# Performance work log

Hardware: AMD Instinct MI355X
Metric: run time of the kernel (lower is better)

## Reference

```python
import jax, jax.numpy as jnp
import numpy as np

N_SRC_F = 40000; N_TGT_F = 40000; N_F = N_SRC_F + N_TGT_F
N_SRC_C = 1024; N_TGT_C = 1024; N_C = N_SRC_C + N_TGT_C
NN = 30        # KPConv neighbors per point
K = 15         # kernel points
C1 = 128       # fine-level feats (first_feats_dim)
C2 = 256       # coarse encoder out dim
GNN = 256      # gnn_feats_dim
HEADS = 4
DGCNN_K = 10
FINAL = 32     # final_feats_dim
EXT_F = 1.0; EXT_C = 2.0   # KPConv influence extents (scaled to unit-cube clouds)
EPS = 1e-12


def kpconv(q_pts, s_pts, s_feats, neighb, kpts, W, extent):
    # q_pts [Nq,3], s_pts [Ns,3], s_feats [Ns,Cin], neighb [Nq,NN], kpts [K,3], W [K,Cin,Cout]
    npts = s_pts[neighb]                              # [Nq,NN,3] irregular gather
    rel = npts - q_pts[:, None, :]
    # ||rel - kp||^2 expanded to avoid a [Nq,NN,K,3] intermediate
    d2 = (jnp.sum(rel * rel, -1)[:, :, None] + jnp.sum(kpts * kpts, -1)[None, None, :]
          - 2.0 * jnp.einsum('njd,kd->njk', rel, kpts))
    infl = jax.nn.relu(1.0 - jnp.sqrt(jnp.maximum(d2, EPS)) / extent)   # [Nq,NN,K]
    nf = s_feats[neighb]                              # [Nq,NN,Cin]
    h = jnp.einsum('njk,njc->nkc', infl, nf)          # kernel-point aggregation
    return jnp.einsum('nkc,kcd->nd', h, W)


def knn_idx(coords, k):
    sq = jnp.sum(coords * coords, -1)
    d2 = sq[:, None] + sq[None, :] - 2.0 * (coords @ coords.T)
    return jax.lax.top_k(-d2, k)[1]


def self_layer(coords, x, W, b):
    # DGCNN edge conv: knn on coords, edge = [x_i, x_j - x_i], 1x1 conv + relu, max over k
    idx = knn_idx(coords, DGCNN_K)
    neigh = x[idx]                                    # [N,k,C]
    ctr = jnp.broadcast_to(x[:, None, :], neigh.shape)
    edge = jnp.concatenate([ctr, neigh - ctr], -1)    # [N,k,2C]
    return jnp.max(jax.nn.relu(edge @ W + b), axis=1)


def cross_layer(x, y, Wq, Wk, Wv, Wm, bm):
    # multi-head cross attention x <- y, residual MLP on [x, message]
    N, C = x.shape
    dh = C // HEADS
    q = (x @ Wq).reshape(N, HEADS, dh)
    k = (y @ Wk).reshape(-1, HEADS, dh)
    v = (y @ Wv).reshape(-1, HEADS, dh)
    attn = jax.nn.softmax(jnp.einsum('nhd,mhd->hnm', q, k) / float(np.sqrt(dh)), axis=-1)
    msg = jnp.einsum('hnm,mhd->nhd', attn, v).reshape(N, C)
    return x + jnp.concatenate([x, msg], -1) @ Wm + bm


def l2norm(x):
    return x / jnp.maximum(jnp.linalg.norm(x, axis=1, keepdims=True), EPS)


def _forward(points_f, points_c, features, kernel_points_f, kernel_points_c,
             W_kp1, W_kp2, W_bottle, b_bottle, W_self1, b_self1,
             Wq, Wk, Wv, W_cross, b_cross, W_self2, b_self2,
             W_proj, b_proj, W_score, b_score, epsilon, W_dec, b_dec,
             neighbors_f, pool_idx, upsample_idx, len_src_c):
    # --- encoder: fine KPConv + strided KPConv to coarse ---
    x_f = kpconv(points_f, points_f, features, neighbors_f, kernel_points_f, W_kp1, EXT_F)  # [N_f,C1]
    skip = x_f
    x_c = kpconv(points_c, points_f, x_f, pool_idx, kernel_points_c, W_kp2, EXT_C)          # [N_c,C2]
    feats_c = x_c @ W_bottle + b_bottle                # bottleneck 1x1 conv -> [N_c,GNN]
    src, tgt = feats_c[:len_src_c], feats_c[len_src_c:]
    sc, tc = points_c[:len_src_c], points_c[len_src_c:]
    # --- GCN: self -> cross -> self (weights shared across src/tgt) ---
    src = self_layer(sc, src, W_self1, b_self1)
    tgt = self_layer(tc, tgt, W_self1, b_self1)
    src2 = cross_layer(src, tgt, Wq, Wk, Wv, W_cross, b_cross)
    tgt2 = cross_layer(tgt, src, Wq, Wk, Wv, W_cross, b_cross)
    src = self_layer(sc, src2, W_self2, b_self2)
    tgt = self_layer(tc, tgt2, W_self2, b_self2)
    feats = jnp.concatenate([src, tgt], 0) @ W_proj + b_proj   # proj_gnn
    scores_c_raw = feats @ W_score + b_score                   # proj_score [N_c,1]
    feats_norm = l2norm(feats)
    # --- bidirectional temperature-softmax matching head ---
    ip = feats_norm[:len_src_c] @ feats_norm[len_src_c:].T     # [Ns,Nt]
    temperature = jnp.exp(epsilon) + 0.03
    s1 = jax.nn.softmax(ip / temperature, axis=1) @ scores_c_raw[len_src_c:]
    s2 = jax.nn.softmax(ip.T / temperature, axis=1) @ scores_c_raw[:len_src_c]
    scores_saliency = jnp.concatenate([s1, s2], 0)
    # condition=True, add_cross_overlap=True branch
    x = jnp.concatenate([scores_c_raw, scores_saliency, feats], 1)    # [N_c, GNN+2]
    # --- decoder: nearest upsample + skip concat + unary conv ---
    x = jnp.concatenate([x[upsample_idx], skip], 1)            # [N_f, GNN+2+C1]
    x = x @ W_dec + b_dec                                      # [N_f, FINAL+2]
    feats_f = l2norm(x[:, :FINAL])
    so = jnp.clip(jax.nn.sigmoid(x[:, FINAL]), 0.0, 1.0)
    ss = jnp.clip(jax.nn.sigmoid(x[:, FINAL + 1]), 0.0, 1.0)
    so = jnp.where(jnp.isnan(so) | jnp.isinf(so), 0.0, so)     # regular_score
    ss = jnp.where(jnp.isnan(ss) | jnp.isinf(ss), 0.0, ss)
    return feats_f, so, ss


def _p(k, shape, fan):
    return jax.random.normal(k, shape, jnp.float32) / float(np.sqrt(fan))


def setup_inputs() -> dict:
    key = jax.random.key(0)
    ks = jax.random.split(key, 24)
    inp = {}
    inp['points_f'] = jax.random.uniform(ks[0], (N_F, 3), jnp.float32)
    inp['points_c'] = jax.random.uniform(ks[1], (N_C, 3), jnp.float32)
    inp['features'] = jnp.ones((N_F, 1), jnp.float32)
    inp['kernel_points_f'] = jax.random.normal(ks[2], (K, 3), jnp.float32) * 0.3
    inp['kernel_points_c'] = jax.random.normal(ks[3], (K, 3), jnp.float32) * 0.6
    inp['W_kp1'] = _p(ks[4], (K, 1, C1), K)
    inp['W_kp2'] = _p(ks[5], (K, C1, C2), K * C1)
    inp['W_bottle'] = _p(ks[6], (C2, GNN), C2); inp['b_bottle'] = jnp.zeros((GNN,), jnp.float32)
    inp['W_self1'] = _p(ks[7], (2 * GNN, GNN), 2 * GNN); inp['b_self1'] = jnp.zeros((GNN,), jnp.float32)
    inp['Wq'] = _p(ks[8], (GNN, GNN), GNN)
    inp['Wk'] = _p(ks[9], (GNN, GNN), GNN)
    inp['Wv'] = _p(ks[10], (GNN, GNN), GNN)
    inp['W_cross'] = _p(ks[11], (2 * GNN, GNN), 2 * GNN); inp['b_cross'] = jnp.zeros((GNN,), jnp.float32)
    inp['W_self2'] = _p(ks[12], (2 * GNN, GNN), 2 * GNN); inp['b_self2'] = jnp.zeros((GNN,), jnp.float32)
    inp['W_proj'] = _p(ks[13], (GNN, GNN), GNN); inp['b_proj'] = jnp.zeros((GNN,), jnp.float32)
    inp['W_score'] = _p(ks[14], (GNN, 1), GNN); inp['b_score'] = jnp.zeros((1,), jnp.float32)
    inp['epsilon'] = jnp.array(-5.0, jnp.float32)
    inp['W_dec'] = _p(ks[15], (GNN + 2 + C1, FINAL + 2), GNN + 2 + C1); inp['b_dec'] = jnp.zeros((FINAL + 2,), jnp.float32)
    inp['neighbors_f'] = jax.random.randint(ks[16], (N_F, NN), 0, N_F)
    inp['pool_idx'] = jax.random.randint(ks[17], (N_C, NN), 0, N_F)
    inp['upsample_idx'] = jax.random.randint(ks[18], (N_F,), 0, N_C)
    inp['len_src_c'] = N_SRC_C
    inp['len_src_f'] = N_SRC_F
    return inp


def reference(points_f, points_c, features, kernel_points_f, kernel_points_c,
              W_kp1, W_kp2, W_bottle, b_bottle, W_self1, b_self1,
              Wq, Wk, Wv, W_cross, b_cross, W_self2, b_self2,
              W_proj, b_proj, W_score, b_score, epsilon, W_dec, b_dec,
              neighbors_f, pool_idx, upsample_idx, len_src_c, len_src_f):
    return _forward(points_f, points_c, features, kernel_points_f, kernel_points_c,
                    W_kp1, W_kp2, W_bottle, b_bottle, W_self1, b_self1,
                    Wq, Wk, Wv, W_cross, b_cross, W_self2, b_self2,
                    W_proj, b_proj, W_score, b_score, epsilon, W_dec, b_dec,
                    neighbors_f, pool_idx, upsample_idx, len_src_c)
```

## Files before the change

### kernel.cpp

```cpp
#include <hip/hip_runtime.h>
#include <math.h>

#define NFINE   80000
#define NCRS    2048
#define NSRC    1024
#define NNB     30
#define KP      15
#define C1D     128
#define C2D     256
#define GD      256
#define DGK     10
#define FINALD  32
#define DECOUT  34

#define NCHUNK  8
#define CHUNK   128
#define TK      8
#define KC      4
#define KSTEP   480
#define GTR     16

__global__ __launch_bounds__(256) void kpconv_fine(
    const float* __restrict__ pts, const float* __restrict__ feat,
    const int* __restrict__ nbr, const float* __restrict__ kp,
    const float* __restrict__ W, float* __restrict__ out)
{
    int t = threadIdx.x, w = t >> 6, lane = t & 63;
    int n = blockIdx.x * 4 + w;
    __shared__ float contrib[4][NNB][17];
    __shared__ float h[4][KP + 1];
    float kx[KP], ky[KP], kz[KP], kk[KP];
#pragma unroll
    for (int k = 0; k < KP; k++) {
        kx[k] = kp[k*3]; ky[k] = kp[k*3+1]; kz[k] = kp[k*3+2];
        kk[k] = kx[k]*kx[k] + ky[k]*ky[k] + kz[k]*kz[k];
    }
    if (lane < NNB) {
        float qx = pts[n*3], qy = pts[n*3+1], qz = pts[n*3+2];
        int id = nbr[n*NNB + lane];
        float rx = pts[id*3]-qx, ry = pts[id*3+1]-qy, rz = pts[id*3+2]-qz;
        float rr = rx*rx + ry*ry + rz*rz;
        float f = feat[id];
#pragma unroll
        for (int k = 0; k < KP; k++) {
            float d2 = rr + kk[k] - 2.f*(rx*kx[k] + ry*ky[k] + rz*kz[k]);
            float infl = fmaxf(1.f - sqrtf(fmaxf(d2, 1e-12f)), 0.f);
            contrib[w][lane][k] = infl * f;
        }
    }
    __syncthreads();
    if (lane < KP) {
        float s = 0.f;
#pragma unroll
        for (int j = 0; j < NNB; j++) s += contrib[w][j][lane];
        h[w][lane] = s;
    }
    __syncthreads();
    float a0 = 0.f, a1 = 0.f;
#pragma unroll
    for (int k = 0; k < KP; k++) {
        float hk = h[w][k];
        a0 += hk * W[k*C1D + lane];
        a1 += hk * W[k*C1D + 64 + lane];
    }
    out[(size_t)n*C1D + lane]      = a0;
    out[(size_t)n*C1D + 64 + lane] = a1;
}

__global__ __launch_bounds__(256) void hh_kernel(
    const float* __restrict__ pc, const float* __restrict__ pf,
    const float* __restrict__ xf, const int* __restrict__ pool,
    const float* __restrict__ kp, float* __restrict__ hhg)
{
    int n = blockIdx.x, t = threadIdx.x;
    __shared__ float kx[KP], ky[KP], kz[KP], kk[KP];
    __shared__ float rel[NNB][4];
    __shared__ int   ids[NNB];
    __shared__ float infl[NNB][KP + 1];
    __shared__ float nf[NNB][C1D];
    if (t < KP) {
        float a = kp[t*3], b = kp[t*3+1], c = kp[t*3+2];
        kx[t] = a; ky[t] = b; kz[t] = c; kk[t] = a*a + b*b + c*c;
    }
    if (t < NNB) {
        int id = pool[n*NNB + t]; ids[t] = id;
        float qx = pc[n*3], qy = pc[n*3+1], qz = pc[n*3+2];
        float rx = pf[id*3]-qx, ry = pf[id*3+1]-qy, rz = pf[id*3+2]-qz;
        rel[t][0] = rx; rel[t][1] = ry; rel[t][2] = rz;
        rel[t][3] = rx*rx + ry*ry + rz*rz;
    }
    __syncthreads();
    for (int i = t; i < NNB*KP; i += 256) {
        int j = i / KP, kq = i % KP;
        float d2 = rel[j][3] + kk[kq]
                 - 2.f*(rel[j][0]*kx[kq] + rel[j][1]*ky[kq] + rel[j][2]*kz[kq]);
        infl[j][kq] = fmaxf(1.f - sqrtf(fmaxf(d2, 1e-12f)) * 0.5f, 0.f);
    }
    for (int i = t; i < NNB*C1D; i += 256) {
        int j = i >> 7, c = i & 127;
        nf[j][c] = xf[(size_t)ids[j]*C1D + c];
    }
    __syncthreads();
    for (int i = t; i < KP*C1D; i += 256) {
        int kq = i >> 7, c = i & 127;
        float s = 0.f;
#pragma unroll
        for (int j = 0; j < NNB; j++) s += infl[j][kq] * nf[j][c];
        hhg[(size_t)n*(KP*C1D) + i] = s;
    }
}

__global__ __launch_bounds__(256) void hh_gemm(
    const float* __restrict__ hhg, const float* __restrict__ W,
    float* __restrict__ pbuf)
{
    int t = threadIdx.x;
    int rg = blockIdx.x >> 2, kc = blockIdx.x & 3;
    int n0 = rg * GTR, kb0 = kc * KSTEP;
    __shared__ float xi[GTR][KSTEP];
    float* xf = &xi[0][0];
    for (int i = t; i < GTR*KSTEP; i += 256) {
        int r = i / KSTEP, c = i - r*KSTEP;
        xf[i] = hhg[(size_t)(n0 + r)*(KP*C1D) + kb0 + c];
    }
    __syncthreads();
    float a[GTR];
#pragma unroll
    for (int r = 0; r < GTR; r++) a[r] = 0.f;
    for (int c = 0; c < KSTEP; c += 4) {
        float w0 = W[(size_t)(kb0+c+0)*C2D + t];
        float w1 = W[(size_t)(kb0+c+1)*C2D + t];
        float w2 = W[(size_t)(kb0+c+2)*C2D + t];
        float w3 = W[(size_t)(kb0+c+3)*C2D + t];
#pragma unroll
        for (int r = 0; r < GTR; r++) {
            float4 xv = *(const float4*)&xi[r][c];
            a[r] += xv.x*w0 + xv.y*w1 + xv.z*w2 + xv.w*w3;
        }
    }
#pragma unroll
    for (int r = 0; r < GTR; r++)
        pbuf[(size_t)kc*NCRS*C2D + (size_t)(n0+r)*C2D + t] = a[r];
}

__global__ __launch_bounds__(256) void bottle_fused(
    const float* __restrict__ pbuf, const float* __restrict__ Wb,
    const float* __restrict__ b, float* __restrict__ out)
{
    int t = threadIdx.x, n0 = blockIdx.x * 4;
    const size_t MN = (size_t)NCRS*C2D;
    __shared__ float xi[4][C2D];
    for (int i = t; i < 4*C2D; i += 256) {
        int r = i >> 8, c = i & 255;
        size_t off = (size_t)(n0+r)*C2D + c;
        xi[r][c] = pbuf[off] + pbuf[MN+off] + pbuf[2*MN+off] + pbuf[3*MN+off];
    }
    __syncthreads();
    float a[4];
#pragma unroll
    for (int r = 0; r < 4; r++) a[r] = 0.f;
    for (int c = 0; c < C2D; c += 4) {
        float w0 = Wb[(c+0)*GD + t];
        float w1 = Wb[(c+1)*GD + t];
        float w2 = Wb[(c+2)*GD + t];
        float w3 = Wb[(c+3)*GD + t];
#pragma unroll
        for (int r = 0; r < 4; r++) {
            float4 xv = *(const float4*)&xi[r][c];
            a[r] += xv.x*w0 + xv.y*w1 + xv.z*w2 + xv.w*w3;
        }
    }
    float bv = b[t];
#pragma unroll
    for (int r = 0; r < 4; r++) out[(size_t)(n0+r)*GD + t] = a[r] + bv;
}

__global__ __launch_bounds__(512) void self_gemm(
    const float* __restrict__ x, const float* __restrict__ W,
    float* __restrict__ Y)
{
    int t = threadIdx.x, n0 = blockIdx.x * 4;
    __shared__ float xi[4][GD];
    for (int i = t; i < 4*GD; i += 512) {
        int r = i >> 8, c = i & 255;
        xi[r][c] = x[(size_t)(n0+r)*GD + c];
    }
    __syncthreads();
    const float* wcol = (t < GD) ? (W + t) : (W + (size_t)GD*GD + (t - GD));
    float a[4];
#pragma unroll
    for (int r = 0; r < 4; r++) a[r] = 0.f;
    for (int c = 0; c < GD; c += 4) {
        float w0 = wcol[(size_t)(c+0)*GD];
        float w1 = wcol[(size_t)(c+1)*GD];
        float w2 = wcol[(size_t)(c+2)*GD];
        float w3 = wcol[(size_t)(c+3)*GD];
#pragma unroll
        for (int r = 0; r < 4; r++) {
            float4 xv = *(const float4*)&xi[r][c];
            a[r] += xv.x*w0 + xv.y*w1 + xv.z*w2 + xv.w*w3;
        }
    }
#pragma unroll
    for (int r = 0; r < 4; r++) Y[(size_t)(n0+r)*512 + t] = a[r];
}

__global__ __launch_bounds__(256) void edge_max(
    const float* __restrict__ Y, const int* __restrict__ knn,
    const float* __restrict__ b, float* __restrict__ out)
{
    int n = blockIdx.x, t = threadIdx.x;
    int base = (n < NSRC) ? 0 : NSRC;
    __shared__ int ids[DGK];
    if (t < DGK) ids[t] = base + knn[n*DGK + t];
    __syncthreads();
    float a  = Y[(size_t)n*512 + t];
    float bn = Y[(size_t)n*512 + GD + t];
    float cst = a - bn + b[t];
    float acc = 0.f;
#pragma unroll
    for (int j = 0; j < DGK; j++) {
        float bj = Y[(size_t)ids[j]*512 + GD + t];
        acc = fmaxf(acc, fmaxf(cst + bj, 0.f));
    }
    out[(size_t)n*GD + t] = acc;
}

__global__ __launch_bounds__(256) void qkv_kernel(
    const float* __restrict__ x, const float* __restrict__ Wq,
    const float* __restrict__ Wk, const float* __restrict__ Wv,
    float* __restrict__ qb, float* __restrict__ kb, float* __restrict__ vb)
{
    int t = threadIdx.x, n0 = blockIdx.x * 4;
    __shared__ float xi[4][GD];
    for (int i = t; i < 4*GD; i += 256) {
        int r = i >> 8, c = i & 255;
        xi[r][c] = x[(size_t)(n0+r)*GD + c];
    }
    __syncthreads();
    const float* Ws[3] = {Wq, Wk, Wv};
    float* outs[3] = {qb, kb, vb};
#pragma unroll
    for (int m = 0; m < 3; m++) {
        const float* W = Ws[m];
        float a[4];
#pragma unroll
        for (int r = 0; r < 4; r++) a[r] = 0.f;
        for (int c = 0; c < GD; c += 4) {
            float w0 = W[(c+0)*GD + t];
            float w1 = W[(c+1)*GD + t];
            float w2 = W[(c+2)*GD + t];
            float w3 = W[(c+3)*GD + t];
#pragma unroll
            for (int r = 0; r < 4; r++) {
                float4 xv = *(const float4*)&xi[r][c];
                a[r] += xv.x*w0 + xv.y*w1 + xv.z*w2 + xv.w*w3;
            }
        }
        float* o = outs[m];
#pragma unroll
        for (int r = 0; r < 4; r++) o[(size_t)(n0+r)*GD + t] = a[r];
    }
}

__global__ __launch_bounds__(256) void knn_kernel(
    const float* __restrict__ pts, int* __restrict__ knn)
{
    int g = blockIdx.x;
    int t = threadIdx.x;
    int base = (g < NSRC) ? 0 : NSRC;
    int local = g - base;
    const float* P = pts + (size_t)base*3;
    __shared__ float d2s[NSRC];
    __shared__ float wval[4];
    __shared__ int   widx[4];
    float qx = P[local*3], qy = P[local*3+1], qz = P[local*3+2];
    float sqn = qx*qx + qy*qy + qz*qz;
#pragma unroll
    for (int ii = 0; ii < 4; ii++) {
        int m = t + ii*256;
        float px = P[m*3], py = P[m*3+1], pz = P[m*3+2];
        float sqm = px*px + py*py + pz*pz;
        d2s[m] = sqn + sqm - 2.f*(qx*px + qy*py + qz*pz);
    }
    __syncthreads();
    for (int r = 0; r < DGK; r++) {
        float bv = 3.4e38f; int bidx = NSRC;
#pragma unroll
        for (int ii = 0; ii < 4; ii++) {
            int m = t + ii*256;
            float v = d2s[m];
            if (v < bv) { bv = v; bidx = m; }
        }
#pragma unroll
        for (int off = 32; off >= 1; off >>= 1) {
            float ov = __shfl_xor(bv, off);
            int   oi = __shfl_xor(bidx, off);
            if (ov < bv || (ov == bv && oi < bidx)) { bv = ov; bidx = oi; }
        }
        if ((t & 63) == 0) { wval[t >> 6] = bv; widx[t >> 6] = bidx; }
        __syncthreads();
        if (t == 0) {
            float fv = wval[0]; int fi = widx[0];
#pragma unroll
            for (int wv2 = 1; wv2 < 4; wv2++)
                if (wval[wv2] < fv || (wval[wv2] == fv && widx[wv2] < fi)) {
                    fv = wval[wv2]; fi = widx[wv2];
                }
            knn[g*DGK + r] = fi;
            d2s[fi] = 3.4e38f;
        }
        __syncthreads();
    }
}

__global__ __launch_bounds__(256) void attn_flash(
    const float* __restrict__ qb, const float* __restrict__ kb,
    const float* __restrict__ vb, float* __restrict__ pm,
    float* __restrict__ pl, float* __restrict__ pacc)
{
    int bidx = blockIdx.x;
    int h = bidx & 3, chunk = (bidx >> 2) & 7, rb = bidx >> 5;
    int t = threadIdx.x;
    int u = t >> 3, li = t & 7;
    int row0 = rb * 128 + u * 4;
    int kbase = (row0 < NSRC) ? NSRC : 0;

    __shared__ float4 kt[2][TK][16];
    __shared__ float4 vt[2][TK][16];

    const float4* kb4 = (const float4*)kb;
    const float4* vb4 = (const float4*)vb;
    size_t gbase = ((size_t)(kbase + chunk*CHUNK)) * 64 + h*16;

    float4 q[4][2];
#pragma unroll
    for (int r = 0; r < 4; r++) {
        const float4* qp = (const float4*)(qb + (size_t)(row0+r)*GD + h*64 + li*8);
        q[r][0] = qp[0]; q[r][1] = qp[1];
    }
    float4 a[4][2];
#pragma unroll
    for (int r = 0; r < 4; r++) {
        a[r][0] = make_float4(0.f,0.f,0.f,0.f);
        a[r][1] = make_float4(0.f,0.f,0.f,0.f);
    }
    float mr[4], lr[4], p[4][TK];
#pragma unroll
    for (int r = 0; r < 4; r++) { mr[r] = -INFINITY; lr[r] = 0.f; }

    int half = t >> 7, sidx = t & 127, skey = sidx >> 4, scomp = sidx & 15;
    const float4* sb = half ? vb4 : kb4;
    float4 rs = sb[gbase + (size_t)skey*64 + scomp];
    if (half) vt[0][skey][scomp] = rs; else kt[0][skey][scomp] = rs;
    __syncthreads();

    const int NT = CHUNK / TK;
    for (int tile = 0; tile < NT; tile++) {
        int cur = tile & 1;
        if (tile + 1 < NT)
            rs = sb[gbase + (size_t)(tile+1)*TK*64 + (size_t)skey*64 + scomp];
        float tm[4];
#pragma unroll
        for (int r = 0; r < 4; r++) tm[r] = -INFINITY;
#pragma unroll
        for (int j = 0; j < TK; j++) {
            float4 k0 = kt[cur][j][li*2+0];
            float4 k1 = kt[cur][j][li*2+1];
#pragma unroll
            for (int r = 0; r < 4; r++) {
                float pp = q[r][0].x*k0.x + q[r][0].y*k0.y + q[r][0].z*k0.z + q[r][0].w*k0.w
                         + q[r][1].x*k1.x + q[r][1].y*k1.y + q[r][1].z*k1.z + q[r][1].w*k1.w;
                pp += __shfl_xor(pp, 1);
                pp += __shfl_xor(pp, 2);
                pp += __shfl_xor(pp, 4);
                pp *= 0.125f;
                p[r][j] = pp;
                tm[r] = fmaxf(tm[r], pp);
            }
        }
#pragma unroll
        for (int r = 0; r < 4; r++) {
            float mn = fmaxf(mr[r], tm[r]);
            float sc = __expf(mr[r] - mn);
            lr[r] *= sc;
            a[r][0].x *= sc; a[r][0].y *= sc; a[r][0].z *= sc; a[r][0].w *= sc;
            a[r][1].x *= sc; a[r][1].y *= sc; a[r][1].z *= sc; a[r][1].w *= sc;
            mr[r] = mn;
        }
#pragma unroll
        for (int j = 0; j < TK; j++) {
            float4 v0 = vt[cur][j][li*2+0];
            float4 v1 = vt[cur][j][li*2+1];
#pragma unroll
            for (int r = 0; r < 4; r++) {
                float e = __expf(p[r][j] - mr[r]);
                lr[r] += e;
                a[r][0].x += e*v0.x; a[r][0].y += e*v0.y;
                a[r][0].z += e*v0.z; a[r][0].w += e*v0.w;
                a[r][1].x += e*v1.x; a[r][1].y += e*v1.y;
                a[r][1].z += e*v1.z; a[r][1].w += e*v1.w;
            }
        }
        if (tile + 1 < NT) {
            __syncthreads();
            if (half) vt[(tile+1)&1][skey][scomp] = rs;
            else      kt[(tile+1)&1][skey][scomp] = rs;
            __syncthreads();
        }
    }
#pragma unroll
    for (int r = 0; r < 4; r++) {
        int pi = (chunk*4 + h)*NCRS + row0 + r;
        if (li == 0) { pm[pi] = mr[r]; pl[pi] = lr[r]; }
        float4* po = (float4*)(pacc + (size_t)pi*64);
        po[li*2+0] = a[r][0];
        po[li*2+1] = a[r][1];
    }
}

__global__ __launch_bounds__(256) void cross_fused(
    const float* __restrict__ x, const float* __restrict__ pm,
    const float* __restrict__ pl, const float* __restrict__ pacc,
    const float* __restrict__ Wm, const float* __restrict__ bm,
    float* __restrict__ out)
{
    int t = threadIdx.x, n0 = blockIdx.x * 4;
    int h = t >> 6, d = t & 63;
    __shared__ float xs[4][GD], ms[4][GD];
    for (int i = t; i < 4*GD; i += 256) {
        int r = i >> 8, c = i & 255;
        xs[r][c] = x[(size_t)(n0+r)*GD + c];
    }
#pragma unroll
    for (int r = 0; r < 4; r++) {
        int row = n0 + r;
        float m = -INFINITY;
#pragma unroll
        for (int c = 0; c < NCHUNK; c++) m = fmaxf(m, pm[(c*4 + h)*NCRS + row]);
        float lsum = 0.f, asum = 0.f;
#pragma unroll
        for (int c = 0; c < NCHUNK; c++) {
            int pi = (c*4 + h)*NCRS + row;
            float w = __expf(pm[pi] - m);
            lsum += pl[pi] * w;
            asum += pacc[(size_t)pi*64 + d] * w;
        }
        ms[r][t] = asum / lsum;
    }
    __syncthreads();
    float bv = bm[t];
    float a[4] = {bv, bv, bv, bv};
    for (int c = 0; c < GD; c += 4) {
        float w10 = Wm[(c+0)*GD + t];
        float w11 = Wm[(c+1)*GD + t];
        float w12 = Wm[(c+2)*GD + t];
        float w13 = Wm[(c+3)*GD + t];
        float w20 = Wm[(GD+c+0)*GD + t];
        float w21 = Wm[(GD+c+1)*GD + t];
        float w22 = Wm[(GD+c+2)*GD + t];
        float w23 = Wm[(GD+c+3)*GD + t];
#pragma unroll
        for (int r = 0; r < 4; r++) {
            float4 xv = *(const float4*)&xs[r][c];
            float4 mv = *(const float4*)&ms[r][c];
            a[r] += xv.x*w10 + xv.y*w11 + xv.z*w12 + xv.w*w13
                  + mv.x*w20 + mv.y*w21 + mv.z*w22 + mv.w*w23;
        }
    }
#pragma unroll
    for (int r = 0; r < 4; r++)
        out[(size_t)(n0+r)*GD + t] = xs[r][t] + a[r];
}

__global__ __launch_bounds__(256) void proj_norm(
    const float* __restrict__ x, const float* __restrict__ W,
    const float* __restrict__ b, const float* __restrict__ Wsc,
    const float* __restrict__ bsc, float* __restrict__ feats,
    float* __restrict__ fnorm, float* __restrict__ scores)
{
    int t = threadIdx.x, n0 = blockIdx.x * 4;
    __shared__ float xi[4][GD];
    __shared__ float pf[4][GD];
    for (int i = t; i < 4*GD; i += 256) {
        int r = i >> 8, c = i & 255;
        xi[r][c] = x[(size_t)(n0+r)*GD + c];
    }
    __syncthreads();
    float a[4] = {0.f, 0.f, 0.f, 0.f};
    for (int c = 0; c < GD; c += 4) {
        float w0 = W[(c+0)*GD + t];
        float w1 = W[(c+1)*GD + t];
        float w2 = W[(c+2)*GD + t];
        float w3 = W[(c+3)*GD + t];
#pragma unroll
        for (int r = 0; r < 4; r++) {
            float4 xv = *(const float4*)&xi[r][c];
            a[r] += xv.x*w0 + xv.y*w1 + xv.z*w2 + xv.w*w3;
        }
    }
    float bv = b[t];
#pragma unroll
    for (int r = 0; r < 4; r++) {
        float v = a[r] + bv;
        feats[(size_t)(n0+r)*GD + t] = v;
        pf[r][t] = v;
    }
    __syncthreads();
    int lane = t & 63, w = t >> 6;
    int rr = n0 + w;
    float q0 = pf[w][lane], q1 = pf[w][64+lane], q2 = pf[w][128+lane], q3 = pf[w][192+lane];
    float sq = q0*q0 + q1*q1 + q2*q2 + q3*q3;
    float sc = q0*Wsc[lane] + q1*Wsc[64+lane] + q2*Wsc[128+lane] + q3*Wsc[192+lane];
#pragma unroll
    for (int off = 32; off >= 1; off >>= 1) {
        sq += __shfl_xor(sq, off);
        sc += __shfl_xor(sc, off);
    }
    float inv = 1.f / fmaxf(sqrtf(sq), 1e-12f);
    fnorm[(size_t)rr*GD + lane]       = q0*inv;
    fnorm[(size_t)rr*GD + 64 + lane]  = q1*inv;
    fnorm[(size_t)rr*GD + 128 + lane] = q2*inv;
    fnorm[(size_t)rr*GD + 192 + lane] = q3*inv;
    if (lane == 0) scores[rr] = sc + bsc[0];
}

__global__ __launch_bounds__(256) void ip_kernel(
    const float* __restrict__ fnorm, float* __restrict__ ip)
{
    int t = threadIdx.x;
    int n0 = (blockIdx.x >> 2) * 4;
    int m  = (blockIdx.x & 3) * 256 + t;
    __shared__ float xs[GD][4];
    for (int i = t; i < 4*GD; i += 256) {
        int r = i >> 8, c = i & 255;
        xs[c][r] = fnorm[(size_t)(n0+r)*GD + c];
    }
    __syncthreads();
    const float4* fr = (const float4*)(fnorm + (size_t)(NSRC + m)*GD);
    float a0 = 0.f, a1 = 0.f, a2 = 0.f, a3 = 0.f;
    for (int c4 = 0; c4 < GD/4; c4++) {
        float4 f = fr[c4];
        float4 xa = *(const float4*)&xs[c4*4+0][0];
        float4 xb = *(const float4*)&xs[c4*4+1][0];
        float4 xc = *(const float4*)&xs[c4*4+2][0];
        float4 xd = *(const float4*)&xs[c4*4+3][0];
        a0 += f.x*xa.x + f.y*xb.x + f.z*xc.x + f.w*xd.x;
        a1 += f.x*xa.y + f.y*xb.y + f.z*xc.y + f.w*xd.y;
        a2 += f.x*xa.z + f.y*xb.z + f.z*xc.z + f.w*xd.z;
        a3 += f.x*xa.w + f.y*xb.w + f.z*xc.w + f.w*xd.w;
    }
    ip[(size_t)(n0+0)*NSRC + m] = a0;
    ip[(size_t)(n0+1)*NSRC + m] = a1;
    ip[(size_t)(n0+2)*NSRC + m] = a2;
    ip[(size_t)(n0+3)*NSRC + m] = a3;
}

__global__ __launch_bounds__(256) void saliency_all(
    const float* __restrict__ ip, const float* __restrict__ scores,
    const float* __restrict__ epsv, float* __restrict__ sal_out)
{
    int g = blockIdx.x, t = threadIdx.x;
    bool col = (g >= NSRC);
    int n = col ? (g - NSRC) : g;
    const float* so = col ? scores : (scores + NSRC);
    float T = expf(epsv[0]) + 0.03f;
    __shared__ float red[256];
    float vals[4];
    float m = -INFINITY;
#pragma unroll
    for (int ii = 0; ii < 4; ii++) {
        int i = t + ii*256;
        float vv = col ? ip[(size_t)i*NSRC + n] : ip[(size_t)n*NSRC + i];
        vv /= T;
        vals[ii] = vv;
        m = fmaxf(m, vv);
    }
    red[t] = m; __syncthreads();
    for (int s = 128; s > 0; s >>= 1) { if (t < s) red[t] = fmaxf(red[t], red[t+s]); __syncthreads(); }
    float mx = red[0]; __syncthreads();
    float se = 0.f, wsum = 0.f;
#pragma unroll
    for (int ii = 0; ii < 4; ii++) {
        int i = t + ii*256;
        float e = expf(vals[ii] - mx);
        se += e; wsum += e * so[i];
    }
    red[t] = se; __syncthreads();
    for (int s = 128; s > 0; s >>= 1) { if (t < s) red[t] += red[t+s]; __syncthreads(); }
    float S = red[0]; __syncthreads();
    red[t] = wsum; __syncthreads();
    for (int s = 128; s > 0; s >>= 1) { if (t < s) red[t] += red[t+s]; __syncthreads(); }
    if (t == 0) sal_out[g] = red[0] / S;
}

__global__ __launch_bounds__(256) void dec_coarse(
    const float* __restrict__ scores, const float* __restrict__ sal,
    const float* __restrict__ feats, const float* __restrict__ Wd,
    const float* __restrict__ bd, float* __restrict__ decfeat)
{
    int t = threadIdx.x, lane = t & 63, w = t >> 6;
    int n = blockIdx.x * 4 + w;
    __shared__ float xr[4][GD];
    for (int c = lane; c < GD; c += 64) xr[w][c] = feats[(size_t)n*GD + c];
    float acc = 0.f;
    if (lane < DECOUT) {
        acc = bd[lane] + scores[n]*Wd[lane] + sal[n]*Wd[DECOUT + lane];
        for (int c = 0; c < GD; c++) acc += xr[w][c] * Wd[(2 + c)*DECOUT + lane];
    }
    if (lane < 40) decfeat[(size_t)n*40 + lane] = (lane < DECOUT) ? acc : 0.f;
}

__global__ __launch_bounds__(256) void decoder_kernel(
    const float* __restrict__ decfeat, const float* __restrict__ skip,
    const int* __restrict__ ups, const float* __restrict__ Wd,
    float* __restrict__ outf, float* __restrict__ outso,
    float* __restrict__ outss)
{
    int t = threadIdx.x;
    __shared__ float wsk[C1D*36];
    for (int i = t; i < C1D*36; i += 256) {
        int cc = i / 36, j = i - cc*36;
        wsk[i] = (j < DECOUT) ? Wd[(size_t)(2 + GD + cc)*DECOUT + j] : 0.f;
    }
    __syncthreads();
    int row = blockIdx.x * 256 + t;
    if (row >= NFINE) return;
    int u = ups[row];
    float4 acc[9];
    const float4* df = (const float4*)(decfeat + (size_t)u*40);
#pragma unroll
    for (int q = 0; q < 9; q++) acc[q] = df[q];
    const float4* sr = (const float4*)(skip + (size_t)row*C1D);
    for (int c4 = 0; c4 < C1D/4; c4++) {
        float4 xv = sr[c4];
        const float* wb = wsk + c4*4*36;
#pragma unroll
        for (int q = 0; q < 9; q++) {
            float4 w0 = *(const float4*)&wb[q*4];
            float4 w1 = *(const float4*)&wb[36 + q*4];
            float4 w2 = *(const float4*)&wb[72 + q*4];
            float4 w3 = *(const float4*)&wb[108 + q*4];
            acc[q].x += xv.x*w0.x + xv.y*w1.x + xv.z*w2.x + xv.w*w3.x;
            acc[q].y += xv.x*w0.y + xv.y*w1.y + xv.z*w2.y + xv.w*w3.y;
            acc[q].z += xv.x*w0.z + xv.y*w1.z + xv.z*w2.z + xv.w*w3.z;
            acc[q].w += xv.x*w0.w + xv.y*w1.w + xv.z*w2.w + xv.w*w3.w;
        }
    }
    float sq = 0.f;
#pragma unroll
    for (int q = 0; q < 8; q++)
        sq += acc[q].x*acc[q].x + acc[q].y*acc[q].y + acc[q].z*acc[q].z + acc[q].w*acc[q].w;
    float inv = 1.f / fmaxf(sqrtf(sq), 1e-12f);
    float4* op = (float4*)(outf + (size_t)row*FINALD);
#pragma unroll
    for (int q = 0; q < 8; q++)
        op[q] = make_float4(acc[q].x*inv, acc[q].y*inv, acc[q].z*inv, acc[q].w*inv);
    float so = 1.f/(1.f + __expf(-acc[8].x));
    so = fminf(fmaxf(so, 0.f), 1.f); if (!(so == so)) so = 0.f;
    float ss = 1.f/(1.f + __expf(-acc[8].y));
    ss = fminf(fmaxf(ss, 0.f), 1.f); if (!(ss == ss)) ss = 0.f;
    outso[row] = so; outss[row] = ss;
}

extern "C" void kernel_launch(void* const* d_in, const int* in_sizes, int n_in,
                              void* d_out, int out_size, void* d_ws, size_t ws_size,
                              hipStream_t stream)
{
    const float* points_f     = (const float*)d_in[0];
    const float* points_c     = (const float*)d_in[1];
    const float* features     = (const float*)d_in[2];
    const float* kp_f         = (const float*)d_in[3];
    const float* kp_c         = (const float*)d_in[4];
    const float* W_kp1        = (const float*)d_in[5];
    const float* W_kp2        = (const float*)d_in[6];
    const float* W_bottle     = (const float*)d_in[7];
    const float* b_bottle     = (const float*)d_in[8];
    const float* W_self1      = (const float*)d_in[9];
    const float* b_self1      = (const float*)d_in[10];
    const float* Wq           = (const float*)d_in[11];
    const float* Wk           = (const float*)d_in[12];
    const float* Wv           = (const float*)d_in[13];
    const float* W_cross      = (const float*)d_in[14];
    const float* b_cross      = (const float*)d_in[15];
    const float* W_self2      = (const float*)d_in[16];
    const float* b_self2      = (const float*)d_in[17];
    const float* W_proj       = (const float*)d_in[18];
    const float* b_proj       = (const float*)d_in[19];
    const float* W_score      = (const float*)d_in[20];
    const float* b_score      = (const float*)d_in[21];
    const float* epsilon      = (const float*)d_in[22];
    const float* W_dec        = (const float*)d_in[23];
    const float* b_dec        = (const float*)d_in[24];
    const int*   neighbors_f  = (const int*)d_in[25];
    const int*   pool_idx     = (const int*)d_in[26];
    const int*   upsample_idx = (const int*)d_in[27];

    float* ws = (float*)d_ws;
    size_t o = 0;
    auto alloc = [&](size_t nfl) { float* p = ws + o; o += (nfl + 63) & ~(size_t)63; return p; };
    float* x_f     = alloc((size_t)NFINE * C1D);
    float* g1      = alloc((size_t)NCRS * GD);
    float* qb      = alloc((size_t)NCRS * GD);
    float* kb      = alloc((size_t)NCRS * GD);
    float* vb      = alloc((size_t)NCRS * GD);
    float* feats_c = alloc((size_t)NCRS * GD);
    float* scores  = alloc(NCRS);
    float* sal     = alloc(NCRS);
    float* decfeat = alloc((size_t)NCRS * 40);
    int*   knn_b   = (int*)alloc(NCRS * DGK);

    const size_t NG = (size_t)NCRS * GD;
    const size_t MN = (size_t)NCRS * C2D;
    const size_t PMN = (size_t)NCRS * 4 * NCHUNK;
    size_t usz = 4*MN + (size_t)NCRS*KP*C1D;
    float* U = alloc(usz);
    float* pbuf = U;
    float* hhg  = U + 4*MN;
    float* Y1   = U;
    float* pm   = U;
    float* pl   = U + PMN;
    float* pacc = U + 2*PMN;
    float* g2   = U + 2*PMN + PMN*64;
    float* Y2   = U;
    float* g3   = U + 2*NG;
    float* feats= U + 3*NG;
    float* fnorm= U + 4*NG;
    float* ip   = U + 5*NG;

    float* outf  = (float*)d_out;
    float* outso = outf + (size_t)NFINE * FINALD;
    float* outss = outso + NFINE;

    kpconv_fine<<<NFINE/4, 256, 0, stream>>>(points_f, features, neighbors_f, kp_f, W_kp1, x_f);
    hh_kernel<<<NCRS, 256, 0, stream>>>(points_c, points_f, x_f, pool_idx, kp_c, hhg);
    hh_gemm<<<(NCRS/GTR)*KC, 256, 0, stream>>>(hhg, W_kp2, pbuf);
    bottle_fused<<<NCRS/4, 256, 0, stream>>>(pbuf, W_bottle, b_bottle, feats_c);

    knn_kernel<<<NCRS, 256, 0, stream>>>(points_c, knn_b);
    self_gemm<<<NCRS/4, 512, 0, stream>>>(feats_c, W_self1, Y1);
    edge_max<<<NCRS, 256, 0, stream>>>(Y1, knn_b, b_self1, g1);
    qkv_kernel<<<NCRS/4, 256, 0, stream>>>(g1, Wq, Wk, Wv, qb, kb, vb);
    attn_flash<<<512, 256, 0, stream>>>(qb, kb, vb, pm, pl, pacc);
    cross_fused<<<NCRS/4, 256, 0, stream>>>(g1, pm, pl, pacc, W_cross, b_cross, g2);
    self_gemm<<<NCRS/4, 512, 0, stream>>>(g2, W_self2, Y2);
    edge_max<<<NCRS, 256, 0, stream>>>(Y2, knn_b, b_self2, g3);

    proj_norm<<<NCRS/4, 256, 0, stream>>>(g3, W_proj, b_proj, W_score, b_score,
                                          feats, fnorm, scores);
    ip_kernel<<<NSRC, 256, 0, stream>>>(fnorm, ip);
    saliency_all<<<NCRS, 256, 0, stream>>>(ip, scores, epsilon, sal);

    dec_coarse<<<NCRS/4, 256, 0, stream>>>(scores, sal, feats, W_dec, b_dec, decfeat);
    decoder_kernel<<<(NFINE + 255)/256, 256, 0, stream>>>(decfeat, x_f, upsample_idx,
                                                          W_dec, outf, outso, outss);
}
```

Before: 462.3 us.

## Merge fine KPConv and coarse kNN into one launch, fold attention scale

```diff
diff --git a/kernel.cpp b/kernel.cpp
--- a/kernel.cpp
+++ b/kernel.cpp
@@ -19,52 +19,110 @@
 #define KC      4
 #define KSTEP   480
 #define GTR     16
-
-__global__ __launch_bounds__(256) void kpconv_fine(
+#define FINEB   10000
+
+__global__ __launch_bounds__(256) void fine_knn(
     const float* __restrict__ pts, const float* __restrict__ feat,
     const int* __restrict__ nbr, const float* __restrict__ kp,
-    const float* __restrict__ W, float* __restrict__ out)
-{
-    int t = threadIdx.x, w = t >> 6, lane = t & 63;
-    int n = blockIdx.x * 4 + w;
-    __shared__ float contrib[4][NNB][17];
-    __shared__ float h[4][KP + 1];
-    float kx[KP], ky[KP], kz[KP], kk[KP];
-#pragma unroll
-    for (int k = 0; k < KP; k++) {
-        kx[k] = kp[k*3]; ky[k] = kp[k*3+1]; kz[k] = kp[k*3+2];
-        kk[k] = kx[k]*kx[k] + ky[k]*ky[k] + kz[k]*kz[k];
-    }
-    if (lane < NNB) {
-        float qx = pts[n*3], qy = pts[n*3+1], qz = pts[n*3+2];
-        int id = nbr[n*NNB + lane];
-        float rx = pts[id*3]-qx, ry = pts[id*3+1]-qy, rz = pts[id*3+2]-qz;
-        float rr = rx*rx + ry*ry + rz*rz;
-        float f = feat[id];
+    const float* __restrict__ W, float* __restrict__ out,
+    const float* __restrict__ pc, int* __restrict__ knn)
+{
+    __shared__ float contrib[8][NNB][17];
+    __shared__ float h[8][KP + 1];
+    __shared__ float d2s[NSRC];
+    __shared__ float wval[4];
+    __shared__ int   widx[4];
+    int t = threadIdx.x;
+    if (blockIdx.x < FINEB) {
+        int w = t >> 6, lane = t & 63;
+        int half = lane >> 5, hl = lane & 31;
+        int pslot = w*2 + half;
+        int n = blockIdx.x * 8 + pslot;
+        float kx[KP], ky[KP], kz[KP], kk[KP];
 #pragma unroll
         for (int k = 0; k < KP; k++) {
-            float d2 = rr + kk[k] - 2.f*(rx*kx[k] + ry*ky[k] + rz*kz[k]);
-            float infl = fmaxf(1.f - sqrtf(fmaxf(d2, 1e-12f)), 0.f);
-            contrib[w][lane][k] = infl * f;
-        }
-    }
-    __syncthreads();
-    if (lane < KP) {
-        float s = 0.f;
-#pragma unroll
-        for (int j = 0; j < NNB; j++) s += contrib[w][j][lane];
-        h[w][lane] = s;
-    }
-    __syncthreads();
-    float a0 = 0.f, a1 = 0.f;
-#pragma unroll
-    for (int k = 0; k < KP; k++) {
-        float hk = h[w][k];
-        a0 += hk * W[k*C1D + lane];
-        a1 += hk * W[k*C1D + 64 + lane];
-    }
-    out[(size_t)n*C1D + lane]      = a0;
-    out[(size_t)n*C1D + 64 + lane] = a1;
+            kx[k] = kp[k*3]; ky[k] = kp[k*3+1]; kz[k] = kp[k*3+2];
+            kk[k] = kx[k]*kx[k] + ky[k]*ky[k] + kz[k]*kz[k];
+        }
+        if (hl < NNB) {
+            float qx = pts[n*3], qy = pts[n*3+1], qz = pts[n*3+2];
+            int id = nbr[n*NNB + hl];
+            float rx = pts[id*3]-qx, ry = pts[id*3+1]-qy, rz = pts[id*3+2]-qz;
+            float rr = rx*rx + ry*ry + rz*rz;
+            float f = feat[id];
+#pragma unroll
+            for (int k = 0; k < KP; k++) {
+                float d2 = rr + kk[k] - 2.f*(rx*kx[k] + ry*ky[k] + rz*kz[k]);
+                float infl = fmaxf(1.f - sqrtf(fmaxf(d2, 1e-12f)), 0.f);
+                contrib[pslot][hl][k] = infl * f;
+            }
+        }
+        __syncthreads();
+        if (hl < KP) {
+            float s = 0.f;
+#pragma unroll
+            for (int j = 0; j < NNB; j++) s += contrib[pslot][j][hl];
+            h[pslot][hl] = s;
+        }
+        __syncthreads();
+        int nA = blockIdx.x * 8 + w*2;
+        float a0 = 0.f, a1 = 0.f, b0 = 0.f, b1 = 0.f;
+#pragma unroll
+        for (int k = 0; k < KP; k++) {
+            float w0 = W[k*C1D + lane];
+            float w1 = W[k*C1D + 64 + lane];
+            float hA = h[w*2][k], hB = h[w*2+1][k];
+            a0 += hA*w0; a1 += hA*w1;
+            b0 += hB*w0; b1 += hB*w1;
+        }
+        out[(size_t)nA*C1D + lane]          = a0;
+        out[(size_t)nA*C1D + 64 + lane]     = a1;
+        out[(size_t)(nA+1)*C1D + lane]      = b0;
+        out[(size_t)(nA+1)*C1D + 64 + lane] = b1;
+    } else {
+        int g = blockIdx.x - FINEB;
+        int base = (g < NSRC) ? 0 : NSRC;
+        int local = g - base;
+        const float* P = pc + (size_t)base*3;
+        float qx = P[local*3], qy = P[local*3+1], qz = P[local*3+2];
+        float sqn = qx*qx + qy*qy + qz*qz;
+#pragma unroll
+        for (int ii = 0; ii < 4; ii++) {
+            int m = t + ii*256;
+            float px = P[m*3], py = P[m*3+1], pz = P[m*3+2];
+            float sqm = px*px + py*py + pz*pz;
+            d2s[m] = sqn + sqm - 2.f*(qx*px + qy*py + qz*pz);
+        }
+        __syncthreads();
+        for (int r = 0; r < DGK; r++) {
+            float bv = 3.4e38f; int bidx = NSRC;
+#pragma unroll
+            for (int ii = 0; ii < 4; ii++) {
+                int m = t + ii*256;
+                float v = d2s[m];
+                if (v < bv) { bv = v; bidx = m; }
+            }
+#pragma unroll
+            for (int off = 32; off >= 1; off >>= 1) {
+                float ov = __shfl_xor(bv, off);
+                int   oi = __shfl_xor(bidx, off);
+                if (ov < bv || (ov == bv && oi < bidx)) { bv = ov; bidx = oi; }
+            }
+            if ((t & 63) == 0) { wval[t >> 6] = bv; widx[t >> 6] = bidx; }
+            __syncthreads();
+            if (t == 0) {
+                float fv = wval[0]; int fi = widx[0];
+#pragma unroll
+                for (int wv2 = 1; wv2 < 4; wv2++)
+                    if (wval[wv2] < fv || (wval[wv2] == fv && widx[wv2] < fi)) {
+                        fv = wval[wv2]; fi = widx[wv2];
+                    }
+                knn[g*DGK + r] = fi;
+                d2s[fi] = 3.4e38f;
+            }
+            __syncthreads();
+        }
+    }
 }
 
 __global__ __launch_bounds__(256) void hh_kernel(
@@ -258,59 +316,9 @@
             }
         }
         float* o = outs[m];
-#pragma unroll
-        for (int r = 0; r < 4; r++) o[(size_t)(n0+r)*GD + t] = a[r];
-    }
-}
-
-__global__ __launch_bounds__(256) void knn_kernel(
-    const float* __restrict__ pts, int* __restrict__ knn)
-{
-    int g = blockIdx.x;
-    int t = threadIdx.x;
-    int base = (g < NSRC) ? 0 : NSRC;
-    int local = g - base;
-    const float* P = pts + (size_t)base*3;
-    __shared__ float d2s[NSRC];
-    __shared__ float wval[4];
-    __shared__ int   widx[4];
-    float qx = P[local*3], qy = P[local*3+1], qz = P[local*3+2];
-    float sqn = qx*qx + qy*qy + qz*qz;
-#pragma unroll
-    for (int ii = 0; ii < 4; ii++) {
-        int m = t + ii*256;
-        float px = P[m*3], py = P[m*3+1], pz = P[m*3+2];
-        float sqm = px*px + py*py + pz*pz;
-        d2s[m] = sqn + sqm - 2.f*(qx*px + qy*py + qz*pz);
-    }
-    __syncthreads();
-    for (int r = 0; r < DGK; r++) {
-        float bv = 3.4e38f; int bidx = NSRC;
-#pragma unroll
-        for (int ii = 0; ii < 4; ii++) {
-            int m = t + ii*256;
-            float v = d2s[m];
-            if (v < bv) { bv = v; bidx = m; }
-        }
-#pragma unroll
-        for (int off = 32; off >= 1; off >>= 1) {
-            float ov = __shfl_xor(bv, off);
-            int   oi = __shfl_xor(bidx, off);
-            if (ov < bv || (ov == bv && oi < bidx)) { bv = ov; bidx = oi; }
-        }
-        if ((t & 63) == 0) { wval[t >> 6] = bv; widx[t >> 6] = bidx; }
-        __syncthreads();
-        if (t == 0) {
-            float fv = wval[0]; int fi = widx[0];
-#pragma unroll
-            for (int wv2 = 1; wv2 < 4; wv2++)
-                if (wval[wv2] < fv || (wval[wv2] == fv && widx[wv2] < fi)) {
-                    fv = wval[wv2]; fi = widx[wv2];
-                }
-            knn[g*DGK + r] = fi;
-            d2s[fi] = 3.4e38f;
-        }
-        __syncthreads();
+        float s = (m == 0) ? 0.125f : 1.f;
+#pragma unroll
+        for (int r = 0; r < 4; r++) o[(size_t)(n0+r)*GD + t] = a[r] * s;
     }
 }
 
@@ -374,19 +382,19 @@
                 pp += __shfl_xor(pp, 1);
                 pp += __shfl_xor(pp, 2);
                 pp += __shfl_xor(pp, 4);
-                pp *= 0.125f;
                 p[r][j] = pp;
                 tm[r] = fmaxf(tm[r], pp);
             }
         }
 #pragma unroll
         for (int r = 0; r < 4; r++) {
-            float mn = fmaxf(mr[r], tm[r]);
-            float sc = __expf(mr[r] - mn);
-            lr[r] *= sc;
-            a[r][0].x *= sc; a[r][0].y *= sc; a[r][0].z *= sc; a[r][0].w *= sc;
-            a[r][1].x *= sc; a[r][1].y *= sc; a[r][1].z *= sc; a[r][1].w *= sc;
-            mr[r] = mn;
+            if (tm[r] > mr[r]) {
+                float sc = __expf(mr[r] - tm[r]);
+                lr[r] *= sc;
+                a[r][0].x *= sc; a[r][0].y *= sc; a[r][0].z *= sc; a[r][0].w *= sc;
+                a[r][1].x *= sc; a[r][1].y *= sc; a[r][1].z *= sc; a[r][1].w *= sc;
+                mr[r] = tm[r];
+            }
         }
 #pragma unroll
         for (int j = 0; j < TK; j++) {
@@ -732,12 +740,12 @@
     float* outso = outf + (size_t)NFINE * FINALD;
     float* outss = outso + NFINE;
 
-    kpconv_fine<<<NFINE/4, 256, 0, stream>>>(points_f, features, neighbors_f, kp_f, W_kp1, x_f);
+    fine_knn<<<FINEB + NCRS, 256, 0, stream>>>(points_f, features, neighbors_f, kp_f,
+                                               W_kp1, x_f, points_c, knn_b);
     hh_kernel<<<NCRS, 256, 0, stream>>>(points_c, points_f, x_f, pool_idx, kp_c, hhg);
     hh_gemm<<<(NCRS/GTR)*KC, 256, 0, stream>>>(hhg, W_kp2, pbuf);
     bottle_fused<<<NCRS/4, 256, 0, stream>>>(pbuf, W_bottle, b_bottle, feats_c);
 
-    knn_kernel<<<NCRS, 256, 0, stream>>>(points_c, knn_b);
     self_gemm<<<NCRS/4, 512, 0, stream>>>(feats_c, W_self1, Y1);
     edge_max<<<NCRS, 256, 0, stream>>>(Y1, knn_b, b_self1, g1);
     qkv_kernel<<<NCRS/4, 256, 0, stream>>>(g1, Wq, Wk, Wv, qb, kb, vb);
```

Result: faster. 432.1 us (-6.5%).
